# Kernel tuning notes

Hardware: AMD Instinct MI355X
Metric: run time of the kernel (lower is better)

Reference implementation:

```python
import jax, jax.numpy as jnp
import numpy as np
from math import pi

TWO_PI = 2.0 * pi

def ringify(x):
    return (x + pi) % TWO_PI - pi

def complex_mean(x, axes):
    dir_x = ringify(jnp.cos(x)).sum(axis=axes)
    dir_y = jnp.sin(x).sum(axis=axes)
    return jnp.arctan2(dir_y, dir_x)

def extract_patches(x, k, s):
    # x: (B, C, H, W) -> (B, Ho, Wo, C, k, k)
    B, C, H, W = x.shape
    Ho = (H - k) // s + 1
    Wo = (W - k) // s + 1
    idx_h = jnp.arange(Ho)[:, None] * s + jnp.arange(k)[None, :]  # (Ho, k)
    idx_w = jnp.arange(Wo)[:, None] * s + jnp.arange(k)[None, :]  # (Wo, k)
    # advanced indexing on dims 2,3 with broadcast shape (Ho, Wo, k, k)
    p = x[:, :, idx_h[:, None, :, None], idx_w[None, :, None, :]]  # (B, C, Ho, Wo, k, k)
    return p.transpose(0, 2, 3, 1, 4, 5)

def ring_conv2d(x, weight, kernel_size, stride):
    # x: (B, C, H, W); weight: (O, C, k, k) -> out: (B, Ho, Wo, O)
    patches = extract_patches(x, kernel_size, stride)            # (B,Ho,Wo,C,k,k)
    w = weight.transpose(1, 2, 3, 0)                              # (C,k,k,O)
    diff = ringify(patches[..., None] - w)                        # (B,Ho,Wo,C,k,k,O)
    return complex_mean(diff, axes=(-4, -3, -2))                  # (B,Ho,Wo,O)

def setup_inputs() -> dict:
    key = jax.random.key(0)
    k1, k2, k3, k4 = jax.random.split(key, 4)
    return {
        "x": jax.random.normal(k1, (4096, 1, 28, 28), dtype=jnp.float32),
        "conv1_weight": jax.random.normal(k2, (4, 1, 2, 2), dtype=jnp.float32),
        "conv2_weight": jax.random.normal(k3, (8, 4, 4, 4), dtype=jnp.float32),
        "ff_weight": jax.random.normal(k4, (288, 10), dtype=jnp.float32),
    }

def reference(x, conv1_weight, conv2_weight, ff_weight):
    h = ringify(x).reshape(-1, 1, 28, 28)
    h = ring_conv2d(h, conv1_weight, kernel_size=2, stride=2)     # (B,14,14,4)
    h = h.transpose(0, 3, 1, 2)                                   # (B,4,14,14)
    h = ring_conv2d(h, conv2_weight, kernel_size=4, stride=2)     # (B,6,6,8)
    h = h.reshape(h.shape[0], -1)                                 # (B,288)
    h = complex_mean(ringify(h[:, :, None] - ff_weight), axes=(-2,))  # (B,10)
    return jnp.sin(h)
```

## Files before the change

kernel.cpp:

```cpp
#include <hip/hip_runtime.h>


typedef _Float16 h2  __attribute__((ext_vector_type(2)));
typedef _Float16 v8h __attribute__((ext_vector_type(8)));
typedef float    f4  __attribute__((ext_vector_type(4)));

__device__ __forceinline__ float fdot2(unsigned a, unsigned b, float c) {
    return __builtin_amdgcn_fdot2(__builtin_bit_cast(h2, a),
                                  __builtin_bit_cast(h2, b), c, false);
}
__device__ __forceinline__ unsigned packh2(float x, float y) {
    h2 h; h.x = (_Float16)x; h.y = (_Float16)y;
    return __builtin_bit_cast(unsigned, h);
}
__device__ __forceinline__ unsigned yrot(unsigned u) {
    return __builtin_amdgcn_alignbit(u, u, 16) ^ 0x8000u;
}

__global__ __launch_bounds__(256) void ringnn_fused(
    const float* __restrict__ x,
    const float* __restrict__ w1,
    const float* __restrict__ w2,
    const float* __restrict__ ffw,
    float* __restrict__ out)
{
    __shared__ __align__(16) unsigned cs1[2][784];
    __shared__ __align__(16) unsigned cs2[2][288];
    __shared__ __align__(16) uint4    b2t[256];
    __shared__ __align__(16) unsigned fft[2880];
    __shared__ uint2 w1t[16];

    const int t    = threadIdx.x;
    const int wave = t >> 6;
    const int lane = t & 63;
    const int img  = t >> 7;
    const int b0   = blockIdx.x * 2;

    const int imA = (t >= 196) ? 1 : 0;
    const int pA  = t - imA * 196;
    const int iA  = pA / 14, jA = pA - iA * 14;
    const float* pxA = x + (b0 + imA) * 784 + (2 * iA) * 28 + 2 * jA;
    const float2 rA0 = *(const float2*)(pxA);
    const float2 rA1 = *(const float2*)(pxA + 28);

    const bool hasB = (t < 136);
    const int pB  = t + 60;
    const int iB  = pB / 14, jB = pB - iB * 14;
    const float* pxB = x + (b0 + 1) * 784 + (2 * iB) * 28 + 2 * jB;
    float2 rB0 = {0.f, 0.f}, rB1 = {0.f, 0.f};
    if (hasB) { rB0 = *(const float2*)(pxB); rB1 = *(const float2*)(pxB + 28); }

    if (t < 16) {
        float s, c;
        __sincosf(w1[t], &s, &c);
        w1t[t] = make_uint2(packh2(c, s), packh2(-s, c));
    }
    {
        const int nn = t & 15;
        const int dy = (t >> 4) & 3;
        const int cc = t >> 6;
        const int o  = nn >> 1;
        unsigned d[4];
        #pragma unroll
        for (int dx = 0; dx < 4; ++dx) {
            float a = w2[o * 64 + cc * 16 + dy * 4 + dx];
            float ss, cw;
            __sincosf(a, &ss, &cw);
            d[dx] = (nn & 1) ? packh2(-ss, cw) : packh2(cw, ss);
        }
        b2t[t] = make_uint4(d[0], d[1], d[2], d[3]);
    }
    for (int e = t; e < 2880; e += 256) {
        float ss, cw;
        __sincosf(ffw[e], &ss, &cw);
        fft[e] = packh2(cw, ss);
    }
    __syncthreads();

    const int n    = lane & 15;
    const int quad = lane >> 4;
    uint4 bf0 = b2t[lane];
    uint4 bf1 = b2t[64 + lane];
    uint4 bf2 = b2t[128 + lane];
    uint4 bf3 = b2t[192 + lane];

    {
        float s0, c0, s1, c1, s2, c2, s3, c3;
        __sincosf(rA0.x, &s0, &c0);
        __sincosf(rA0.y, &s1, &c1);
        __sincosf(rA1.x, &s2, &c2);
        __sincosf(rA1.y, &s3, &c3);
        const unsigned u0 = packh2(c0, s0), u1 = packh2(c1, s1);
        const unsigned u2 = packh2(c2, s2), u3 = packh2(c3, s3);
        #pragma unroll
        for (int o = 0; o < 4; ++o) {
            const uint2 wa = w1t[o * 4 + 0], wb = w1t[o * 4 + 1];
            const uint2 wc = w1t[o * 4 + 2], wd = w1t[o * 4 + 3];
            float X = 0.f, Y = 0.f;
            X = fdot2(u0, wa.x, X); Y = fdot2(u0, wa.y, Y);
            X = fdot2(u1, wb.x, X); Y = fdot2(u1, wb.y, Y);
            X = fdot2(u2, wc.x, X); Y = fdot2(u2, wc.y, Y);
            X = fdot2(u3, wd.x, X); Y = fdot2(u3, wd.y, Y);
            const float rinv = rsqrtf(fmaxf(fmaf(X, X, Y * Y), 1e-30f));
            cs1[imA][o * 196 + pA] = packh2(X * rinv, Y * rinv);
        }
    }
    if (hasB) {
        float s0, c0, s1, c1, s2, c2, s3, c3;
        __sincosf(rB0.x, &s0, &c0);
        __sincosf(rB0.y, &s1, &c1);
        __sincosf(rB1.x, &s2, &c2);
        __sincosf(rB1.y, &s3, &c3);
        const unsigned u0 = packh2(c0, s0), u1 = packh2(c1, s1);
        const unsigned u2 = packh2(c2, s2), u3 = packh2(c3, s3);
        #pragma unroll
        for (int o = 0; o < 4; ++o) {
            const uint2 wa = w1t[o * 4 + 0], wb = w1t[o * 4 + 1];
            const uint2 wc = w1t[o * 4 + 2], wd = w1t[o * 4 + 3];
            float X = 0.f, Y = 0.f;
            X = fdot2(u0, wa.x, X); Y = fdot2(u0, wa.y, Y);
            X = fdot2(u1, wb.x, X); Y = fdot2(u1, wb.y, Y);
            X = fdot2(u2, wc.x, X); Y = fdot2(u2, wc.y, Y);
            X = fdot2(u3, wd.x, X); Y = fdot2(u3, wd.y, Y);
            const float rinv = rsqrtf(fmaxf(fmaf(X, X, Y * Y), 1e-30f));
            cs1[1][o * 196 + pB] = packh2(X * rinv, Y * rinv);
        }
    }
    __syncthreads();

    const unsigned* c1 = &cs1[0][0];
    for (int tile = wave; tile < 5; tile += 4) {
        const int p  = tile * 16 + n;
        const int pc = (p < 72) ? p : 71;
        const int im = (pc >= 36) ? 1 : 0;
        const int ps = pc - im * 36;
        const int i  = ps / 6;
        const int j  = ps - i * 6;
        const unsigned base = (unsigned)(im * 784 + (2 * i + quad) * 14 + 2 * j);
        f4 acc = {0.f, 0.f, 0.f, 0.f};
        #pragma unroll
        for (int c = 0; c < 4; ++c) {
            uint2 lo = *(const uint2*)(c1 + base + c * 196);
            uint2 hi = *(const uint2*)(c1 + base + c * 196 + 2);
            uint4 a4 = make_uint4(lo.x, lo.y, hi.x, hi.y);
            v8h av = __builtin_bit_cast(v8h, a4);
            v8h bv = __builtin_bit_cast(v8h, (c == 0) ? bf0 : (c == 1) ? bf1
                                              : (c == 2) ? bf2 : bf3);
            acc = __builtin_amdgcn_mfma_f32_16x16x32_f16(av, bv, acc, 0, 0, 0);
        }
        float pr0 = __shfl_xor(acc[0], 1);
        float pr1 = __shfl_xor(acc[1], 1);
        float pr2 = __shfl_xor(acc[2], 1);
        float pr3 = __shfl_xor(acc[3], 1);
        if (!(n & 1)) {
            const int o = n >> 1;
            float Xs[4] = {acc[0], acc[1], acc[2], acc[3]};
            float Ys[4] = {pr0, pr1, pr2, pr3};
            #pragma unroll
            for (int r = 0; r < 4; ++r) {
                const int p2 = tile * 16 + quad * 4 + r;
                if (p2 < 72) {
                    const int im2 = (p2 >= 36) ? 1 : 0;
                    const int ps2 = p2 - im2 * 36;
                    float X = Xs[r], Y = Ys[r];
                    float rinv = rsqrtf(fmaxf(fmaf(X, X, Y * Y), 1e-30f));
                    cs2[im2][ps2 * 8 + o] = packh2(X * rinv, Y * rinv);
                }
            }
        }
    }
    __syncthreads();

    {
        const int half = wave & 1;
        const int nl   = lane / 12;
        const int g    = lane - nl * 12;
        float XA = 0.f, YA = 0.f, XB = 0.f, YB = 0.f;
        if (nl < 5) {
            const int n3 = half * 5 + nl;
            #pragma unroll 6
            for (int k = 0; k < 12; ++k) {
                const int fA = g + 12 * k;
                const int fB = fA + 144;
                unsigned va = cs2[img][fA];
                unsigned vb = cs2[img][fB];
                unsigned ua = fft[fA * 10 + n3];
                unsigned ub = fft[fB * 10 + n3];
                XA = fdot2(va, ua, XA);
                YA = fdot2(va, yrot(ua), YA);
                XB = fdot2(vb, ub, XB);
                YB = fdot2(vb, yrot(ub), YB);
            }
        }
        float X = XA + XB, Y = YA + YB;
        float qX = X + __shfl_down(X, 4) + __shfl_down(X, 8);
        float qY = Y + __shfl_down(Y, 4) + __shfl_down(Y, 8);
        float sX = qX + __shfl_down(qX, 1) + __shfl_down(qX, 2) + __shfl_down(qX, 3);
        float sY = qY + __shfl_down(qY, 1) + __shfl_down(qY, 2) + __shfl_down(qY, 3);
        if (g == 0 && nl < 5) {
            const int n3 = half * 5 + nl;
            float rinv = rsqrtf(fmaxf(fmaf(sX, sX, sY * sY), 1e-30f));
            out[(b0 + img) * 10 + n3] = sY * rinv;
        }
    }
}

extern "C" void kernel_launch(void* const* d_in, const int* in_sizes, int n_in,
                              void* d_out, int out_size, void* d_ws, size_t ws_size,
                              hipStream_t stream) {
    const float* x   = (const float*)d_in[0];
    const float* w1  = (const float*)d_in[1];
    const float* w2  = (const float*)d_in[2];
    const float* ffw = (const float*)d_in[3];
    (void)d_ws; (void)ws_size;
    ringnn_fused<<<2048, 256, 0, stream>>>(x, w1, w2, ffw, (float*)d_out);
}
```

Baseline: 78.17 us.

## Process four images per 512-thread block and alias weight tables in LDS

Doubles the block to 512 threads handling four images, so each block's per-block weight preprocessing (sincos of the ff, conv2 and conv1 weights) is shared across twice as many images. The conv2 B-fragment table is aliased into the ff-weight LDS buffer, and the ff table is now built after conv2 completes, which keeps shared memory per block low. This reduces redundant transcendental work per image. The cost is larger blocks, tighter occupancy granularity, and an extra ordering dependency between the stages.

```diff
diff --git a/kernel.cpp b/kernel.cpp
--- a/kernel.cpp
+++ b/kernel.cpp
@@ -17,45 +17,42 @@
     return __builtin_amdgcn_alignbit(u, u, 16) ^ 0x8000u;
 }
 
-__global__ __launch_bounds__(256) void ringnn_fused(
+__global__ __launch_bounds__(512) void ringnn_fused(
     const float* __restrict__ x,
     const float* __restrict__ w1,
     const float* __restrict__ w2,
     const float* __restrict__ ffw,
     float* __restrict__ out)
 {
-    __shared__ __align__(16) unsigned cs1[2][784];
-    __shared__ __align__(16) unsigned cs2[2][288];
-    __shared__ __align__(16) uint4    b2t[256];
-    __shared__ __align__(16) unsigned fft[2880];
+    __shared__ __align__(16) unsigned cs1[4][784];
+    __shared__ __align__(16) unsigned cs2[4][288];
+    __shared__ __align__(16) unsigned fftb[2880];
     __shared__ uint2 w1t[16];
 
     const int t    = threadIdx.x;
     const int wave = t >> 6;
     const int lane = t & 63;
-    const int img  = t >> 7;
-    const int b0   = blockIdx.x * 2;
-
-    const int imA = (t >= 196) ? 1 : 0;
-    const int pA  = t - imA * 196;
+    const int b0   = blockIdx.x * 4;
+
+    const int pAi = t;
+    const int imA = pAi / 196;
+    const int pA  = pAi - imA * 196;
     const int iA  = pA / 14, jA = pA - iA * 14;
     const float* pxA = x + (b0 + imA) * 784 + (2 * iA) * 28 + 2 * jA;
     const float2 rA0 = *(const float2*)(pxA);
     const float2 rA1 = *(const float2*)(pxA + 28);
 
-    const bool hasB = (t < 136);
-    const int pB  = t + 60;
+    const bool hasB = (t < 272);
+    const int pBi = t + 512;
+    const int imB = pBi / 196;
+    const int pB  = pBi - imB * 196;
     const int iB  = pB / 14, jB = pB - iB * 14;
-    const float* pxB = x + (b0 + 1) * 784 + (2 * iB) * 28 + 2 * jB;
+    const float* pxB = x + (b0 + imB) * 784 + (2 * iB) * 28 + 2 * jB;
     float2 rB0 = {0.f, 0.f}, rB1 = {0.f, 0.f};
     if (hasB) { rB0 = *(const float2*)(pxB); rB1 = *(const float2*)(pxB + 28); }
 
-    if (t < 16) {
-        float s, c;
-        __sincosf(w1[t], &s, &c);
-        w1t[t] = make_uint2(packh2(c, s), packh2(-s, c));
-    }
-    {
+    uint4* b2t = (uint4*)fftb;
+    if (t < 256) {
         const int nn = t & 15;
         const int dy = (t >> 4) & 3;
         const int cc = t >> 6;
@@ -70,10 +67,10 @@
         }
         b2t[t] = make_uint4(d[0], d[1], d[2], d[3]);
     }
-    for (int e = t; e < 2880; e += 256) {
-        float ss, cw;
-        __sincosf(ffw[e], &ss, &cw);
-        fft[e] = packh2(cw, ss);
+    if (t < 16) {
+        float s, c;
+        __sincosf(w1[t], &s, &c);
+        w1t[t] = make_uint2(packh2(c, s), packh2(-s, c));
     }
     __syncthreads();
 
@@ -123,17 +120,16 @@
             X = fdot2(u2, wc.x, X); Y = fdot2(u2, wc.y, Y);
             X = fdot2(u3, wd.x, X); Y = fdot2(u3, wd.y, Y);
             const float rinv = rsqrtf(fmaxf(fmaf(X, X, Y * Y), 1e-30f));
-            cs1[1][o * 196 + pB] = packh2(X * rinv, Y * rinv);
+            cs1[imB][o * 196 + pB] = packh2(X * rinv, Y * rinv);
         }
     }
     __syncthreads();
 
     const unsigned* c1 = &cs1[0][0];
-    for (int tile = wave; tile < 5; tile += 4) {
+    for (int tile = wave; tile < 9; tile += 8) {
         const int p  = tile * 16 + n;
-        const int pc = (p < 72) ? p : 71;
-        const int im = (pc >= 36) ? 1 : 0;
-        const int ps = pc - im * 36;
+        const int im = p / 36;
+        const int ps = p - im * 36;
         const int i  = ps / 6;
         const int j  = ps - i * 6;
         const unsigned base = (unsigned)(im * 784 + (2 * i + quad) * 14 + 2 * j);
@@ -158,20 +154,24 @@
             float Ys[4] = {pr0, pr1, pr2, pr3};
             #pragma unroll
             for (int r = 0; r < 4; ++r) {
-                const int p2 = tile * 16 + quad * 4 + r;
-                if (p2 < 72) {
-                    const int im2 = (p2 >= 36) ? 1 : 0;
-                    const int ps2 = p2 - im2 * 36;
-                    float X = Xs[r], Y = Ys[r];
-                    float rinv = rsqrtf(fmaxf(fmaf(X, X, Y * Y), 1e-30f));
-                    cs2[im2][ps2 * 8 + o] = packh2(X * rinv, Y * rinv);
-                }
+                const int p2  = tile * 16 + quad * 4 + r;
+                const int im2 = p2 / 36;
+                const int ps2 = p2 - im2 * 36;
+                float X = Xs[r], Y = Ys[r];
+                float rinv = rsqrtf(fmaxf(fmaf(X, X, Y * Y), 1e-30f));
+                cs2[im2][ps2 * 8 + o] = packh2(X * rinv, Y * rinv);
             }
         }
     }
+    for (int e = t; e < 2880; e += 512) {
+        float ss, cw;
+        __sincosf(ffw[e], &ss, &cw);
+        fftb[e] = packh2(cw, ss);
+    }
     __syncthreads();
 
     {
+        const int img3 = wave >> 1;
         const int half = wave & 1;
         const int nl   = lane / 12;
         const int g    = lane - nl * 12;
@@ -182,10 +182,10 @@
             for (int k = 0; k < 12; ++k) {
                 const int fA = g + 12 * k;
                 const int fB = fA + 144;
-                unsigned va = cs2[img][fA];
-                unsigned vb = cs2[img][fB];
-                unsigned ua = fft[fA * 10 + n3];
-                unsigned ub = fft[fB * 10 + n3];
+                unsigned va = cs2[img3][fA];
+                unsigned vb = cs2[img3][fB];
+                unsigned ua = fftb[fA * 10 + n3];
+                unsigned ub = fftb[fB * 10 + n3];
                 XA = fdot2(va, ua, XA);
                 YA = fdot2(va, yrot(ua), YA);
                 XB = fdot2(vb, ub, XB);
@@ -200,7 +200,7 @@
         if (g == 0 && nl < 5) {
             const int n3 = half * 5 + nl;
             float rinv = rsqrtf(fmaxf(fmaf(sX, sX, sY * sY), 1e-30f));
-            out[(b0 + img) * 10 + n3] = sY * rinv;
+            out[(b0 + img3) * 10 + n3] = sY * rinv;
         }
     }
 }
@@ -213,5 +213,5 @@
     const float* w2  = (const float*)d_in[2];
     const float* ffw = (const float*)d_in[3];
     (void)d_ws; (void)ws_size;
-    ringnn_fused<<<2048, 256, 0, stream>>>(x, w1, w2, ffw, (float*)d_out);
-}
+    ringnn_fused<<<1024, 512, 0, stream>>>(x, w1, w2, ffw, (float*)d_out);
+}
```

Result: faster. 73.23 us (-6.3%).
